# Kernel tuning notes

Hardware: AMD Instinct MI355X
Metric: run time of the kernel (lower is better)

The kernel has to match this reference:

```python
import jax, jax.numpy as jnp
import numpy as np

VOCAB = 50000
D = 200          # word_dimension
A = 32           # aspect_dimension
NUM_NEG = 5
AVG_RATING = 3.5
LR_RATING = 1.0
LR_ABAE = 1.0
N = 4096         # reviews in batch
L = 128          # tokens per review
B = 1024         # users / items
H = 16           # avg history length (flat = B*H)


def setup_inputs() -> dict:
    key = jax.random.key(0)
    ks = jax.random.split(key, 12)
    hist = jax.random.randint(ks[0], (N, L), 0, VOCAB)
    rev_pos = jax.random.normal(ks[1], (N, D), jnp.float32)
    rev_neg = jax.random.normal(ks[2], (N * NUM_NEG, D), jnp.float32)
    user = jax.random.randint(ks[3], (B,), 0, B)
    item = jax.random.randint(ks[4], (B,), 0, B)
    label = jax.random.uniform(ks[5], (B,), jnp.float32) * 4.0 + 1.0
    user_hist_idx = jax.random.randint(ks[6], (B * H,), 0, N)
    item_hist_idx = jax.random.randint(ks[7], (B * H,), 0, N)
    # segment ids: each user/item owns H consecutive entries (ragged in general)
    user_seg_ids = jnp.repeat(jnp.arange(B), H)
    item_seg_ids = jnp.repeat(jnp.arange(B), H)
    word_emb = jax.random.normal(ks[8], (VOCAB, D), jnp.float32) * 0.1
    M_w = jax.random.normal(ks[9], (D, D), jnp.float32) * (1.0 / np.sqrt(D))
    W_w = jax.random.normal(ks[10], (A, D), jnp.float32) * (1.0 / np.sqrt(D))
    W_b = jnp.zeros((A,), jnp.float32)
    T_w = jax.random.normal(ks[11], (D, A), jnp.float32) * (1.0 / np.sqrt(A))
    return {
        'historical_review': hist, 'review_positive': rev_pos,
        'review_negative': rev_neg, 'user': user, 'item': item,
        'label': label, 'user_hist_idx': user_hist_idx,
        'user_seg_ids': user_seg_ids, 'item_hist_idx': item_hist_idx,
        'item_seg_ids': item_seg_ids, 'word_emb': word_emb,
        'M_w': M_w, 'W_w': W_w, 'W_b': W_b, 'T_w': T_w,
    }


def _l2norm(x, axis):
    # matches F.normalize(p=2, eps=1e-12)
    n = jnp.sqrt(jnp.sum(x * x, axis=axis, keepdims=True))
    return x / jnp.maximum(n, 1e-12)


def reference(historical_review, review_positive, review_negative, user, item,
              label, user_hist_idx, user_seg_ids, item_hist_idx, item_seg_ids,
              word_emb, M_w, W_w, W_b, T_w):
    n, l = historical_review.shape
    d = word_emb.shape[1]
    e_w = word_emb[historical_review]                       # [N,L,D]
    # dx = (e_w @ M^T) . y_s  -> attention logits over tokens
    dx = jnp.einsum('nld,nd->nl', e_w @ M_w.T, review_positive)
    ax = jax.nn.softmax(dx, axis=1)                          # [N,L]
    # NOTE: original uses .view(N, D, L) (a reshape, NOT a transpose) -- faithful
    z_s = jnp.einsum('ndl,nl->nd', e_w.reshape(n, d, l), ax)  # [N,D]
    p_t = jax.nn.softmax(z_s @ W_w.T + W_b, axis=1)          # [N,A]
    r_s = p_t @ T_w.T                                        # [N,D]

    c1 = jnp.sum(_l2norm(r_s, 1) * _l2norm(z_s, 1), axis=-1)  # [N]
    c1r = jnp.repeat(c1, NUM_NEG)                            # [N*NUM_NEG]
    z_n = review_negative.reshape(n, NUM_NEG, d)
    c2 = jnp.sum(_l2norm(z_n, 2) * _l2norm(r_s, 1)[:, None, :], axis=-1).reshape(-1)
    # MarginRankingLoss(margin=0, target=1): mean(max(0, c2 - c1))
    J_loss = jnp.mean(jnp.maximum(0.0, c2 - c1r))
    Tn = _l2norm(T_w, 0)                                     # normalize columns
    U_loss = jnp.mean((Tn.T @ Tn - jnp.eye(A, dtype=T_w.dtype)) ** 2)
    abae_loss = U_loss + J_loss

    nb = label.shape[0]
    def seg_mean(idx, seg):
        g = r_s[idx]                                         # ragged gather [F,D]
        s = jax.ops.segment_sum(g, seg, num_segments=nb)
        c = jax.ops.segment_sum(jnp.ones(idx.shape[0], r_s.dtype), seg, num_segments=nb)
        return s / c[:, None]

    u_emb = seg_mean(user_hist_idx, user_seg_ids)            # [B,D]
    i_emb = seg_mean(item_hist_idx, item_seg_ids)            # [B,D]
    prediction = jnp.sum(u_emb * i_emb, axis=-1) + AVG_RATING
    rating_loss = jnp.mean((prediction - label) ** 2)
    obj = LR_RATING * rating_loss + LR_ABAE * abae_loss
    return (obj, rating_loss, abae_loss)
```

## Files before the change

kernel.cpp:

```cpp
#include <hip/hip_runtime.h>

#define NN 4096
#define LL 128
#define DD 200
#define AA 32
#define NEG 5
#define BB 1024

#define WS_RS    0
#define WS_ACC   (NN*DD)

template<int C, int RM>
__device__ __forceinline__ float dpp_add(float v){
  int t = __builtin_amdgcn_update_dpp(0, __float_as_int(v), C, RM, 0xf, false);
  return v + __int_as_float(t);
}
template<int C, int RM>
__device__ __forceinline__ float dpp_fmax(float v){
  int t = __builtin_amdgcn_update_dpp(__float_as_int(-3.0e38f), __float_as_int(v),
                                      C, RM, 0xf, false);
  return fmaxf(v, __int_as_float(t));
}
__device__ __forceinline__ float sum64(float v){
  v = dpp_add<0xB1, 0xF>(v);
  v = dpp_add<0x4E, 0xF>(v);
  v = dpp_add<0x124,0xF>(v);
  v = dpp_add<0x128,0xF>(v);
  v = dpp_add<0x142,0xA>(v);
  v = dpp_add<0x143,0xC>(v);
  return v;
}
__device__ __forceinline__ float max64(float v){
  v = dpp_fmax<0xB1, 0xF>(v);
  v = dpp_fmax<0x4E, 0xF>(v);
  v = dpp_fmax<0x124,0xF>(v);
  v = dpp_fmax<0x128,0xF>(v);
  v = dpp_fmax<0x142,0xA>(v);
  v = dpp_fmax<0x143,0xC>(v);
  return v;
}
__device__ __forceinline__ float sum8(float v){
  v = dpp_add<0xB1, 0xF>(v);
  v = dpp_add<0x4E, 0xF>(v);
  v = dpp_add<0x124,0xF>(v);
  return v;
}
__device__ __forceinline__ float rdlane(float v, int l){
  return __int_as_float(__builtin_amdgcn_readlane(__float_as_int(v), l));
}
__device__ __forceinline__ float dot4(float4 a, float4 b){
  return a.x*b.x + a.y*b.y + a.z*b.z + a.w*b.w;
}

__device__ __forceinline__ void z_load(float4* buf, const float* __restrict__ we,
                                       const int* hrowl, int d2, int q){
  unsigned f0 = (unsigned)d2 * 128u + 4u * (unsigned)q;
#pragma unroll
  for (int i = 0; i < 4; ++i){
    unsigned f = f0 + 32u * i;
    unsigned r = f / 200u;
    buf[i] = *(const float4*)(we + (size_t)hrowl[r] * DD + (f - r * 200u));
  }
}
__device__ __forceinline__ float z_red(const float4* buf, const float4* ax){
  return dot4(buf[0],ax[0]) + dot4(buf[1],ax[1]) + dot4(buf[2],ax[2]) + dot4(buf[3],ax[3]);
}

__global__ __launch_bounds__(256, 5)
void k_main(const int* __restrict__ hist, const float* __restrict__ rev_pos,
            const float* __restrict__ rev_neg, const float* __restrict__ word_emb,
            const float* __restrict__ M_w, const float* __restrict__ W_w,
            const float* __restrict__ W_b, const float* __restrict__ T_w,
            float* __restrict__ rs_out, float* __restrict__ acc)
{
  __shared__ __align__(16) float smem[1704];
  float* y_l  = smem;
  float* dxax = smem + 208;
  float* zsm  = smem + 336;
  float* r_l  = smem + 536;
  float* lsps = smem + 736;
  float* sc   = smem + 768;
  int*   hrowl= (int*)(smem + 776);
  float* ypart= smem + 904;

  const int n = blockIdx.x;
  const int t = threadIdx.x;
  const int w = t >> 6, j = t & 63;
  const int wu = __builtin_amdgcn_readfirstlane(w);

  if (t < DD) r_l[t] = rev_pos[(size_t)n * DD + t];
  if (t < LL) hrowl[t] = hist[(size_t)n * LL + t];

  const int* hrow_g = hist + (size_t)n * LL + 32 * wu;
  const int col = (j < 50) ? 4 * j : 0;
  int rA[8], rB[8];
  float4 gA[8], gB[8];
#pragma unroll
  for (int i = 0; i < 8; ++i) rA[i] = hrow_g[i];
#pragma unroll
  for (int i = 0; i < 8; ++i)
    gA[i] = *(const float4*)(word_emb + (size_t)rA[i] * DD + col);
#pragma unroll
  for (int i = 0; i < 8; ++i) rB[i] = hrow_g[8 + i];
#pragma unroll
  for (int i = 0; i < 8; ++i)
    gB[i] = *(const float4*)(word_emb + (size_t)rB[i] * DD + col);

  __syncthreads();

  if (j < 50){
    float ax = 0.f, ay = 0.f, az = 0.f, aw = 0.f;
    const float* Mb = M_w + (50 * wu) * DD + 4 * j;
    const float* rb = r_l + 50 * wu;
#pragma unroll 10
    for (int dk = 0; dk < 50; ++dk){
      float rv = rb[dk];
      float4 m4 = *(const float4*)(Mb + dk * DD);
      ax = fmaf(rv, m4.x, ax); ay = fmaf(rv, m4.y, ay);
      az = fmaf(rv, m4.z, az); aw = fmaf(rv, m4.w, aw);
    }
    float4 o; o.x = ax; o.y = ay; o.z = az; o.w = aw;
    *(float4*)(ypart + wu * 200 + 4 * j) = o;
  }
  __syncthreads();
  if (t < DD) y_l[t] = ypart[t] + ypart[200 + t] + ypart[400 + t] + ypart[600 + t];
  __syncthreads();

  {
    float4 y4 = make_float4(0.f, 0.f, 0.f, 0.f);
    if (j < 50) y4 = *(const float4*)(y_l + 4 * j);
#pragma unroll
    for (int i = 0; i < 8; ++i){
      float v = sum64(dot4(gA[i], y4));
      if (j == 63) dxax[32 * wu + i] = v;
    }
#pragma unroll
    for (int i = 0; i < 8; ++i) rA[i] = hrow_g[16 + i];
#pragma unroll
    for (int i = 0; i < 8; ++i)
      gA[i] = *(const float4*)(word_emb + (size_t)rA[i] * DD + col);
#pragma unroll
    for (int i = 0; i < 8; ++i){
      float v = sum64(dot4(gB[i], y4));
      if (j == 63) dxax[32 * wu + 8 + i] = v;
    }
#pragma unroll
    for (int i = 0; i < 8; ++i) rB[i] = hrow_g[24 + i];
#pragma unroll
    for (int i = 0; i < 8; ++i)
      gB[i] = *(const float4*)(word_emb + (size_t)rB[i] * DD + col);
#pragma unroll
    for (int i = 0; i < 8; ++i){
      float v = sum64(dot4(gA[i], y4));
      if (j == 63) dxax[32 * wu + 16 + i] = v;
    }
#pragma unroll
    for (int i = 0; i < 8; ++i){
      float v = sum64(dot4(gB[i], y4));
      if (j == 63) dxax[32 * wu + 24 + i] = v;
    }
  }

  const int q = j & 7, oct = j >> 3;
  int d2c[7];
#pragma unroll
  for (int k = 0; k < 7; ++k){
    int off = 8 * k + oct;
    d2c[k] = 50 * wu + (off < 50 ? off : 49);
  }
  float4 za[4], zb[4];
  z_load(za, word_emb, hrowl, d2c[0], q);
  z_load(zb, word_emb, hrowl, d2c[1], q);

  __syncthreads();

  if (w == 0){
    float a0 = dxax[j], a1 = dxax[j + 64];
    float M = rdlane(max64(fmaxf(a0, a1)), 63);
    float e0 = __expf(a0 - M), e1 = __expf(a1 - M);
    float S = rdlane(sum64(e0 + e1), 63);
    float inv = 1.f / S;
    dxax[j] = e0 * inv; dxax[j + 64] = e1 * inv;
  }
  __syncthreads();

  {
    float4 axr[4];
    axr[0] = *(const float4*)(dxax +      4 * q);
    axr[1] = *(const float4*)(dxax + 32 + 4 * q);
    axr[2] = *(const float4*)(dxax + 64 + 4 * q);
    axr[3] = *(const float4*)(dxax + 96 + 4 * q);
    float v;
    v = sum8(z_red(za, axr)); if (q == 0) zsm[d2c[0]] = v;
    z_load(za, word_emb, hrowl, d2c[2], q);
    v = sum8(z_red(zb, axr)); if (q == 0) zsm[d2c[1]] = v;
    z_load(zb, word_emb, hrowl, d2c[3], q);
    v = sum8(z_red(za, axr)); if (q == 0) zsm[d2c[2]] = v;
    z_load(za, word_emb, hrowl, d2c[4], q);
    v = sum8(z_red(zb, axr)); if (q == 0) zsm[d2c[3]] = v;
    z_load(zb, word_emb, hrowl, d2c[5], q);
    v = sum8(z_red(za, axr)); if (q == 0) zsm[d2c[4]] = v;
    z_load(za, word_emb, hrowl, d2c[6], q);
    v = sum8(z_red(zb, axr)); if (q == 0) zsm[d2c[5]] = v;
    v = sum8(z_red(za, axr)); if (q == 0 && oct < 2) zsm[d2c[6]] = v;
  }
  __syncthreads();

#pragma unroll
  for (int aa = 0; aa < 8; ++aa){
    int a = wu * 8 + aa;
    const float* Wr = W_w + a * DD;
    float p = zsm[j] * Wr[j] + zsm[j + 64] * Wr[j + 64] + zsm[j + 128] * Wr[j + 128];
    if (j < 8) p += zsm[j + 192] * Wr[j + 192];
    float v = sum64(p);
    if (j == 63) lsps[a] = v + W_b[a];
  }
  __syncthreads();

  if (w == 0){
    float v = (j < 32) ? lsps[j] : -3.0e38f;
    float M = rdlane(max64(v), 63);
    float e = __expf(v - M);
    float S = rdlane(sum64(e), 63);
    if (j < 32) lsps[j] = e / S;
  }
  __syncthreads();

  if (t < DD){
    const float4* Tq = (const float4*)(T_w + t * AA);
    float a = 0.f;
#pragma unroll
    for (int q8 = 0; q8 < 8; ++q8){
      float4 tv = Tq[q8];
      a += lsps[4*q8]*tv.x + lsps[4*q8+1]*tv.y + lsps[4*q8+2]*tv.z + lsps[4*q8+3]*tv.w;
    }
    r_l[t] = a;
    rs_out[(size_t)n * DD + t] = a;
  }
  __syncthreads();

  if (w == 0){
    float rr = 0, zz = 0, rz = 0;
    if (j < 50){
      float4 rv = *(float4*)(r_l + 4 * j);
      float4 zv = *(float4*)(zsm + 4 * j);
      rr = dot4(rv, rv); zz = dot4(zv, zv); rz = dot4(rv, zv);
    }
    rr = rdlane(sum64(rr), 63); zz = rdlane(sum64(zz), 63); rz = rdlane(sum64(rz), 63);
    if (j == 0){
      float nr = fmaxf(sqrtf(rr), 1e-12f);
      float nz = fmaxf(sqrtf(zz), 1e-12f);
      sc[0] = rz / (nr * nz);
      sc[1] = nr;
    }
  }
  __syncthreads();

  for (int g5 = w; g5 < NEG; g5 += 4){
    const float* neg = rev_neg + ((size_t)n * NEG + g5) * DD;
    float nn = 0, dr = 0;
    if (j < 50){
      float4 v = *(const float4*)(neg + 4 * j);
      float4 rv = *(float4*)(r_l + 4 * j);
      nn = dot4(v, v); dr = dot4(v, rv);
    }
    nn = rdlane(sum64(nn), 63); dr = rdlane(sum64(dr), 63);
    if (j == 0){
      float c2 = dr / (fmaxf(sqrtf(nn), 1e-12f) * sc[1]);
      sc[2 + g5] = fmaxf(0.f, c2 - sc[0]);
    }
  }
  __syncthreads();
  if (t == 0) atomicAdd(&acc[0], sc[2] + sc[3] + sc[4] + sc[5] + sc[6]);
}

__device__ __forceinline__ void finalize(float* acc, float* out){
  float R = atomicAdd(&acc[2], 0.f) / (float)BB;
  float J = atomicAdd(&acc[0], 0.f) / (float)(NN * NEG);
  float U = atomicAdd(&acc[1], 0.f);
  out[0] = R + U + J;
  out[1] = R;
  out[2] = U + J;
}

__global__ __launch_bounds__(256)
void k_tail(const int* __restrict__ u_idx, const int* __restrict__ i_idx,
            const float* __restrict__ rs, const float* __restrict__ label,
            const float* __restrict__ T_w, float* __restrict__ acc,
            float* __restrict__ out){
  __shared__ __align__(16) float smem[6500];
  const int b = blockIdx.x, t = threadIdx.x, w = t >> 6, j = t & 63;

  if (b == BB){
    float* Tl  = smem;
    float* nrm = smem + 6464;
    float* wred= smem + 6496;
    for (int i = t; i < DD * AA; i += 256){
      int d = i >> 5, a = i & 31;
      Tl[a * 202 + d] = T_w[i];
    }
    __syncthreads();
    if (t < AA){
      float s = 0.f;
      for (int d = 0; d < DD; d += 2){
        float2 v = *(float2*)&Tl[t * 202 + d];
        s += v.x * v.x + v.y * v.y;
      }
      nrm[t] = fmaxf(sqrtf(s), 1e-12f);
    }
    __syncthreads();
    int a = t >> 3, b0 = (t & 7) * 4;
    float d0 = 0, d1 = 0, d2 = 0, d3 = 0;
    for (int d = 0; d < DD; d += 2){
      float2 va = *(float2*)&Tl[a * 202 + d];
      float2 v0 = *(float2*)&Tl[(b0    ) * 202 + d];
      float2 v1 = *(float2*)&Tl[(b0 + 1) * 202 + d];
      float2 v2 = *(float2*)&Tl[(b0 + 2) * 202 + d];
      float2 v3 = *(float2*)&Tl[(b0 + 3) * 202 + d];
      d0 += va.x * v0.x + va.y * v0.y;
      d1 += va.x * v1.x + va.y * v1.y;
      d2 += va.x * v2.x + va.y * v2.y;
      d3 += va.x * v3.x + va.y * v3.y;
    }
    float na = nrm[a], gg = 0.f, g;
    g = d0 / (na * nrm[b0    ]) - (a == b0     ? 1.f : 0.f); gg += g * g;
    g = d1 / (na * nrm[b0 + 1]) - (a == b0 + 1 ? 1.f : 0.f); gg += g * g;
    g = d2 / (na * nrm[b0 + 2]) - (a == b0 + 2 ? 1.f : 0.f); gg += g * g;
    g = d3 / (na * nrm[b0 + 3]) - (a == b0 + 3 ? 1.f : 0.f); gg += g * g;
    float v = sum64(gg);
    if (j == 63) wred[w] = v;
    __syncthreads();
    if (t == 0){
      atomicAdd(&acc[1], (wred[0] + wred[1] + wred[2] + wred[3]) / (float)(AA * AA));
      __threadfence();
      int prev = atomicAdd((int*)acc + 8, 1);
      if (prev == BB) finalize(acc, out);
    }
    return;
  }

  int*   idxs = (int*)smem;
  float* wred = smem + 32;
  if (t < 16) idxs[t] = u_idx[b * 16 + t];
  else if (t < 32) idxs[t] = i_idx[b * 16 + (t - 16)];
  __syncthreads();
  float su = 0.f, si = 0.f;
  if (t < DD){
#pragma unroll
    for (int k = 0; k < 16; ++k) su += rs[(size_t)idxs[k] * DD + t];
#pragma unroll
    for (int k = 0; k < 16; ++k) si += rs[(size_t)idxs[16 + k] * DD + t];
  }
  float v = sum64(su * si);
  if (j == 63) wred[w] = v;
  __syncthreads();
  if (t == 0){
    float dot = wred[0] + wred[1] + wred[2] + wred[3];
    float pred = dot * (1.f / 256.f) + 3.5f;
    float e = pred - label[b];
    atomicAdd(&acc[2], e * e);
    __threadfence();
    int prev = atomicAdd((int*)acc + 8, 1);
    if (prev == BB) finalize(acc, out);
  }
}

extern "C" void kernel_launch(void* const* d_in, const int* in_sizes, int n_in,
                              void* d_out, int out_size, void* d_ws, size_t ws_size,
                              hipStream_t stream){
  const int*   hist     = (const int*)  d_in[0];
  const float* rev_pos  = (const float*)d_in[1];
  const float* rev_neg  = (const float*)d_in[2];
  const float* label    = (const float*)d_in[5];
  const int*   u_idx    = (const int*)  d_in[6];
  const int*   i_idx    = (const int*)  d_in[8];
  const float* word_emb = (const float*)d_in[10];
  const float* M_w      = (const float*)d_in[11];
  const float* W_w      = (const float*)d_in[12];
  const float* W_b      = (const float*)d_in[13];
  const float* T_w      = (const float*)d_in[14];

  float* ws   = (float*)d_ws;
  float* rs   = ws + WS_RS;
  float* accp = ws + WS_ACC;

  hipMemsetAsync(accp, 0, 64, stream);
  k_main<<<NN, 256, 0, stream>>>(hist, rev_pos, rev_neg, word_emb, M_w,
                                 W_w, W_b, T_w, rs, accp);
  k_tail<<<BB + 1, 256, 0, stream>>>(u_idx, i_idx, rs, label, T_w, accp,
                                     (float*)d_out);
}
```

Before: 318.8 us.

## Defer embedding gathers, compute softmax redundantly per wave, raise occupancy

Moves the first word-embedding gathers after the M·r projection so they are not held in registers across that phase, and raises the launch-bounds occupancy hint from 5 to 7 blocks per CU. The attention softmax is now recomputed by every wave and applied on the fly, which removes one barrier and a shared-memory write-back. The T_w rows are prefetched before the aspect softmax barrier. The risks are lost latency hiding for the early gathers, possible register spills under the tighter bound, and duplicated exp work in every wave.

```diff
diff --git a/kernel.cpp b/kernel.cpp
--- a/kernel.cpp
+++ b/kernel.cpp
@@ -51,6 +51,12 @@
 __device__ __forceinline__ float dot4(float4 a, float4 b){
   return a.x*b.x + a.y*b.y + a.z*b.z + a.w*b.w;
 }
+__device__ __forceinline__ float4 smx4(float4 r, float M, float invS){
+  float4 o;
+  o.x = __expf(r.x - M) * invS; o.y = __expf(r.y - M) * invS;
+  o.z = __expf(r.z - M) * invS; o.w = __expf(r.w - M) * invS;
+  return o;
+}
 
 __device__ __forceinline__ void z_load(float4* buf, const float* __restrict__ we,
                                        const int* hrowl, int d2, int q){
@@ -66,7 +72,7 @@
   return dot4(buf[0],ax[0]) + dot4(buf[1],ax[1]) + dot4(buf[2],ax[2]) + dot4(buf[3],ax[3]);
 }
 
-__global__ __launch_bounds__(256, 5)
+__global__ __launch_bounds__(256, 7)
 void k_main(const int* __restrict__ hist, const float* __restrict__ rev_pos,
             const float* __restrict__ rev_neg, const float* __restrict__ word_emb,
             const float* __restrict__ M_w, const float* __restrict__ W_w,
@@ -90,22 +96,6 @@
 
   if (t < DD) r_l[t] = rev_pos[(size_t)n * DD + t];
   if (t < LL) hrowl[t] = hist[(size_t)n * LL + t];
-
-  const int* hrow_g = hist + (size_t)n * LL + 32 * wu;
-  const int col = (j < 50) ? 4 * j : 0;
-  int rA[8], rB[8];
-  float4 gA[8], gB[8];
-#pragma unroll
-  for (int i = 0; i < 8; ++i) rA[i] = hrow_g[i];
-#pragma unroll
-  for (int i = 0; i < 8; ++i)
-    gA[i] = *(const float4*)(word_emb + (size_t)rA[i] * DD + col);
-#pragma unroll
-  for (int i = 0; i < 8; ++i) rB[i] = hrow_g[8 + i];
-#pragma unroll
-  for (int i = 0; i < 8; ++i)
-    gB[i] = *(const float4*)(word_emb + (size_t)rB[i] * DD + col);
-
   __syncthreads();
 
   if (j < 50){
@@ -126,9 +116,31 @@
   if (t < DD) y_l[t] = ypart[t] + ypart[200 + t] + ypart[400 + t] + ypart[600 + t];
   __syncthreads();
 
+  const int q = j & 7, oct = j >> 3;
+  int d2c[7];
+#pragma unroll
+  for (int k = 0; k < 7; ++k){
+    int off = 8 * k + oct;
+    d2c[k] = 50 * wu + (off < 50 ? off : 49);
+  }
+  float4 za[4], zb[4];
   {
     float4 y4 = make_float4(0.f, 0.f, 0.f, 0.f);
-    if (j < 50) y4 = *(const float4*)(y_l + 4 * j);
+    int col = 0;
+    if (j < 50){ y4 = *(const float4*)(y_l + 4 * j); col = 4 * j; }
+    const int* hrow_g = hist + (size_t)n * LL + 32 * wu;
+    int rA[8], rB[8];
+    float4 gA[8], gB[8];
+#pragma unroll
+    for (int i = 0; i < 8; ++i) rA[i] = hrow_g[i];
+#pragma unroll
+    for (int i = 0; i < 8; ++i)
+      gA[i] = *(const float4*)(word_emb + (size_t)rA[i] * DD + col);
+#pragma unroll
+    for (int i = 0; i < 8; ++i) rB[i] = hrow_g[8 + i];
+#pragma unroll
+    for (int i = 0; i < 8; ++i)
+      gB[i] = *(const float4*)(word_emb + (size_t)rB[i] * DD + col);
 #pragma unroll
     for (int i = 0; i < 8; ++i){
       float v = sum64(dot4(gA[i], y4));
@@ -149,6 +161,8 @@
 #pragma unroll
     for (int i = 0; i < 8; ++i)
       gB[i] = *(const float4*)(word_emb + (size_t)rB[i] * DD + col);
+    z_load(za, word_emb, hrowl, d2c[0], q);
+    z_load(zb, word_emb, hrowl, d2c[1], q);
 #pragma unroll
     for (int i = 0; i < 8; ++i){
       float v = sum64(dot4(gA[i], y4));
@@ -160,36 +174,22 @@
       if (j == 63) dxax[32 * wu + 24 + i] = v;
     }
   }
-
-  const int q = j & 7, oct = j >> 3;
-  int d2c[7];
-#pragma unroll
-  for (int k = 0; k < 7; ++k){
-    int off = 8 * k + oct;
-    d2c[k] = 50 * wu + (off < 50 ? off : 49);
-  }
-  float4 za[4], zb[4];
-  z_load(za, word_emb, hrowl, d2c[0], q);
-  z_load(zb, word_emb, hrowl, d2c[1], q);
-
-  __syncthreads();
-
-  if (w == 0){
+  __syncthreads();
+
+  float smM, smInv;
+  {
     float a0 = dxax[j], a1 = dxax[j + 64];
-    float M = rdlane(max64(fmaxf(a0, a1)), 63);
-    float e0 = __expf(a0 - M), e1 = __expf(a1 - M);
-    float S = rdlane(sum64(e0 + e1), 63);
-    float inv = 1.f / S;
-    dxax[j] = e0 * inv; dxax[j + 64] = e1 * inv;
-  }
-  __syncthreads();
+    smM = rdlane(max64(fmaxf(a0, a1)), 63);
+    float S = rdlane(sum64(__expf(a0 - smM) + __expf(a1 - smM)), 63);
+    smInv = 1.f / S;
+  }
 
   {
     float4 axr[4];
-    axr[0] = *(const float4*)(dxax +      4 * q);
-    axr[1] = *(const float4*)(dxax + 32 + 4 * q);
-    axr[2] = *(const float4*)(dxax + 64 + 4 * q);
-    axr[3] = *(const float4*)(dxax + 96 + 4 * q);
+    axr[0] = smx4(*(const float4*)(dxax +      4 * q), smM, smInv);
+    axr[1] = smx4(*(const float4*)(dxax + 32 + 4 * q), smM, smInv);
+    axr[2] = smx4(*(const float4*)(dxax + 64 + 4 * q), smM, smInv);
+    axr[3] = smx4(*(const float4*)(dxax + 96 + 4 * q), smM, smInv);
     float v;
     v = sum8(z_red(za, axr)); if (q == 0) zsm[d2c[0]] = v;
     z_load(za, word_emb, hrowl, d2c[2], q);
@@ -215,6 +215,13 @@
     float v = sum64(p);
     if (j == 63) lsps[a] = v + W_b[a];
   }
+
+  float4 Tq[8];
+  if (t < DD){
+    const float4* Tp = (const float4*)(T_w + t * AA);
+#pragma unroll
+    for (int q8 = 0; q8 < 8; ++q8) Tq[q8] = Tp[q8];
+  }
   __syncthreads();
 
   if (w == 0){
@@ -227,7 +234,6 @@
   __syncthreads();
 
   if (t < DD){
-    const float4* Tq = (const float4*)(T_w + t * AA);
     float a = 0.f;
 #pragma unroll
     for (int q8 = 0; q8 < 8; ++q8){
```

After: 357.5 us. 1.12x slower.
